# Kernel optimization log

Hardware: AMD Instinct MI355X
Metric: run time of the kernel (lower is better)

Reference implementation:

```python
import jax, jax.numpy as jnp
import numpy as np

B, L, D_IN = 16, 2048, 512
HID, H = 512, 8
D = HID // H          # head dim
FACTOR = 5
U = min(FACTOR * int(np.ceil(np.log(L))), L)  # u_q == u_k == 40 (L == S)


def setup_inputs() -> dict:
    key = jax.random.key(0)
    ks = jax.random.split(key, 8)
    s = 1.0 / np.sqrt(D_IN).astype(np.float32)
    return {
        "q_in": jax.random.normal(ks[0], (B, L, D_IN), jnp.float32),
        "k_in": jax.random.normal(ks[1], (B, L, D_IN), jnp.float32),
        "v_in": jax.random.normal(ks[2], (B, L, D_IN), jnp.float32),
        "Wq": jax.random.normal(ks[3], (D_IN, HID), jnp.float32) * s,
        "Wk": jax.random.normal(ks[4], (D_IN, HID), jnp.float32) * s,
        "Wv": jax.random.normal(ks[5], (D_IN, HID), jnp.float32) * s,
        "Wo": jax.random.normal(ks[6], (HID, HID // H), jnp.float32) / np.sqrt(HID).astype(np.float32),
        "indx_q_seq": jax.random.randint(ks[7], (L,), 0, L, dtype=jnp.int32),
    }


def reference(q_in, k_in, v_in, Wq, Wk, Wv, Wo, indx_q_seq):
    # projections + (memory-reinterpreting, as in the TF source) head reshape
    q = (q_in @ Wq).reshape(B, H, L, D)
    k = (k_in @ Wk).reshape(B, H, L, D)
    v = (v_in @ Wv).reshape(B, H, L, D)

    # --- _prob_qk ---
    # TF's chained gathers on the broadcast k_expand collapse to pairing
    # query s with the single key indx_q_seq[s]; all sample_k columns of
    # Q_K_sample are identical, so M = max - sum/L = dot * (1 - U/L).
    k_sel = k[:, :, indx_q_seq, :]                        # [B,H,L,D]
    dot = jnp.einsum('bhle,bhle->bhl', q, k_sel)          # [B,H,L]
    M = dot - dot * (jnp.float32(U) / jnp.float32(L))
    _, m_top = jax.lax.top_k(M, U)                        # [B,H,U]

    b_idx = jnp.arange(B)[:, None, None]
    h_idx = jnp.arange(H)[None, :, None]
    q_red = q[b_idx, h_idx, m_top]                        # [B,H,U,D]
    scores = jnp.einsum('bhue,bhle->bhul', q_red, k)      # [B,H,U,L]
    scores = scores * (1.0 / np.sqrt(D).astype(np.float32))

    # --- initial context: causal cumsum of values ---
    context = jnp.cumsum(v, axis=-2)                      # [B,H,L,D]

    # --- update context at the top-U query positions (causal mask) ---
    causal = jnp.arange(L)[None, None, None, :] > m_top[..., None]
    scores = jnp.where(causal, -jnp.inf, scores)
    attn = jax.nn.softmax(scores, axis=-1)                # [B,H,U,L]
    upd = jnp.einsum('bhul,bhld->bhud', attn, v)          # [B,H,U,D]
    context = context.at[b_idx, h_idx, m_top].set(upd)

    out = context.reshape(B, L, HID) @ Wo                 # [B,L,HID//H]
    return out
```

## Files before the change

### kernel.cpp

```cpp
#include <hip/hip_runtime.h>
#include <hip/hip_bf16.h>
#include <math.h>

#define B_   16
#define L_   2048
#define DIN  512
#define HID_ 512
#define H_   8
#define D_   64
#define U_   40
#define BH   (B_*H_)

typedef unsigned short u16;
typedef unsigned int u32;
typedef unsigned long long u64;
typedef __bf16 bf16x8 __attribute__((ext_vector_type(8)));
typedef float f32x4 __attribute__((ext_vector_type(4)));

__device__ __forceinline__ u16 f2bf(float x) {
  __bf16 b = (__bf16)x;
  return __builtin_bit_cast(unsigned short, b);
}
__device__ __forceinline__ float bf2f(u16 h) {
  return __uint_as_float(((unsigned)h) << 16);
}
__device__ __forceinline__ float bflo(u32 x) { return __uint_as_float(x << 16); }
__device__ __forceinline__ float bfhi(u32 x) { return __uint_as_float(x & 0xFFFF0000u); }
__device__ __forceinline__ u32 pk2(float a, float b) {
  return (u32)f2bf(a) | ((u32)f2bf(b) << 16);
}
__device__ __forceinline__ void gload16(const u16* g, u16* l) {
  __builtin_amdgcn_global_load_lds(
      (__attribute__((address_space(1))) void*)(g),
      (__attribute__((address_space(3))) void*)(l), 16, 0, 0);
}
__device__ __forceinline__ u64 mkkey(float Mv, int l) {
  u32 fb = __float_as_uint(Mv);
  u32 mapped = (fb & 0x80000000u) ? ~fb : (fb | 0x80000000u);
  return ((u64)mapped << 32) | (u64)(0xFFFFFFFFu - (u32)l);
}

__global__ __launch_bounds__(256)
void wsplit_kernel(const float* __restrict__ W, u16* __restrict__ Bt) {
  int tid = blockIdx.x * 256 + threadIdx.x;
  int n = tid & 511, k = tid >> 9;
  float a = W[(size_t)k * 512 + n];
  u16 hi = f2bf(a);
  u16 lo = f2bf(a - bf2f(hi));
  int kb = k >> 5, kc = k & 31;
  int slotH = kc >> 3, wi = kc & 7;
  int swzH = (slotH     ^ (n & 7)) << 3;
  int swzL = ((4+slotH) ^ (n & 7)) << 3;
  Bt[(size_t)n * 1024 + kb * 64 + swzH + wi] = hi;
  Bt[(size_t)n * 1024 + kb * 64 + swzL + wi] = lo;
}

template<int NPASS>
__global__ __launch_bounds__(256, 4)
void gemm_proj(const float* __restrict__ A, const u16* __restrict__ Bt,
               float* __restrict__ C) {
  __shared__ u16 As[128 * 64];
  __shared__ u16 Bs[128 * 64];
  const int t = threadIdx.x;
  const int w = t >> 6, lane = t & 63;
  const int lhi = lane >> 4, l16 = lane & 15;
  const int row0 = blockIdx.x * 128, col0 = blockIdx.y * 128;
  const int wrow = (w >> 1) * 64, wcol = (w & 1) * 64;

  const u16* gB = Bt + (size_t)(col0 + w * 32 + (lane >> 3)) * 1024 + (lane & 7) * 8;
  u16* lB = &Bs[(w * 32) * 64];

  f32x4 acc[4][4];
  #pragma unroll
  for (int i = 0; i < 4; ++i)
    #pragma unroll
    for (int j = 0; j < 4; ++j) acc[i][j] = (f32x4){0.f, 0.f, 0.f, 0.f};

  for (int kb = 0; kb < 16; ++kb) {
    #pragma unroll
    for (int i = 0; i < 4; ++i)
      gload16(gB + kb * 64 + (size_t)i * 8 * 1024, lB + i * 8 * 64);
    #pragma unroll
    for (int i = 0; i < 4; ++i) {
      int r  = (t >> 3) + 32 * i;
      int c4 = (t & 7) * 4;
      float4 v = *reinterpret_cast<const float4*>(
          &A[(size_t)(row0 + r) * 512 + kb * 32 + c4]);
      ushort4 h4;
      h4.x = f2bf(v.x); h4.y = f2bf(v.y); h4.z = f2bf(v.z); h4.w = f2bf(v.w);
      int slotH = c4 >> 3, wi = c4 & 7;
      int baseH = r * 64 + (((slotH)     ^ (r & 7)) << 3) + wi;
      *reinterpret_cast<ushort4*>(&As[baseH]) = h4;
      if constexpr (NPASS == 3) {
        ushort4 lo4;
        lo4.x = f2bf(v.x - bf2f(h4.x)); lo4.y = f2bf(v.y - bf2f(h4.y));
        lo4.z = f2bf(v.z - bf2f(h4.z)); lo4.w = f2bf(v.w - bf2f(h4.w));
        int baseL = r * 64 + (((4 + slotH) ^ (r & 7)) << 3) + wi;
        *reinterpret_cast<ushort4*>(&As[baseL]) = lo4;
      }
    }
    __syncthreads();

#define PASS(APART, BPART)                                                      \
    { bf16x8 af[4], bfr[4];                                                     \
      _Pragma("unroll") for (int i = 0; i < 4; ++i) {                           \
        int ra = wrow + i * 16 + l16;                                           \
        af[i] = *reinterpret_cast<const bf16x8*>(                               \
            &As[ra * 64 + ((((APART) + lhi) ^ (ra & 7)) << 3)]); }              \
      _Pragma("unroll") for (int j = 0; j < 4; ++j) {                           \
        int cb = wcol + j * 16 + l16;                                           \
        bfr[j] = *reinterpret_cast<const bf16x8*>(                              \
            &Bs[cb * 64 + ((((BPART) + lhi) ^ (cb & 7)) << 3)]); }              \
      _Pragma("unroll") for (int i = 0; i < 4; ++i)                             \
        _Pragma("unroll") for (int j = 0; j < 4; ++j)                           \
          acc[i][j] = __builtin_amdgcn_mfma_f32_16x16x32_bf16(                  \
              af[i], bfr[j], acc[i][j], 0, 0, 0); }

    PASS(0, 0)
    if constexpr (NPASS == 3) {
      PASS(0, 4)
      PASS(4, 0)
    }
#undef PASS
    __syncthreads();
  }
  #pragma unroll
  for (int i = 0; i < 4; ++i)
    #pragma unroll
    for (int j = 0; j < 4; ++j)
      #pragma unroll
      for (int r = 0; r < 4; ++r)
        C[(size_t)(row0 + wrow + i * 16 + lhi * 4 + r) * 512
          + col0 + wcol + j * 16 + l16] = acc[i][j][r];
}

__global__ __launch_bounds__(256)
void dotsel_kernel(const float* __restrict__ qp, const float* __restrict__ kp,
                   const int* __restrict__ indx, u64* __restrict__ cand) {
  __shared__ u64 keys[256];
  __shared__ u64 wmax[4];
  const int bh = blockIdx.x, ch = blockIdx.y;
  const int t = threadIdx.x, w = t >> 6, lane = t & 63;
  const size_t boff = (size_t)bh * 131072;
  const int l0 = ch * 256 + w * 64;
  const float cUL = 40.0f / 2048.0f;

  for (int i = 0; i < 64; i += 4) {
    float p[4];
    #pragma unroll
    for (int jj = 0; jj < 4; ++jj) {
      int l = l0 + i + jj;
      int ls = indx[l];
      p[jj] = qp[boff + (size_t)l * 64 + lane] * kp[boff + (size_t)ls * 64 + lane];
    }
    #pragma unroll
    for (int off = 32; off >= 1; off >>= 1)
      #pragma unroll
      for (int jj = 0; jj < 4; ++jj) p[jj] += __shfl_xor(p[jj], off, 64);
    if (lane == 0) {
      #pragma unroll
      for (int jj = 0; jj < 4; ++jj) {
        float Mv = p[jj] - p[jj] * cUL;
        keys[w * 64 + i + jj] = mkkey(Mv, l0 + i + jj);
      }
    }
  }
  __syncthreads();

  u64 myk = keys[t];
  for (int u = 0; u < U_; ++u) {
    u64 b = myk;
    #pragma unroll
    for (int off = 32; off >= 1; off >>= 1) {
      u64 v = __shfl_xor(b, off, 64);
      if (v > b) b = v;
    }
    if (lane == 0) wmax[w] = b;
    __syncthreads();
    u64 m = wmax[0];
    if (wmax[1] > m) m = wmax[1];
    if (wmax[2] > m) m = wmax[2];
    if (wmax[3] > m) m = wmax[3];
    if (myk == m) myk = 0;
    if (t == 0) cand[((size_t)(bh * 8 + ch)) * U_ + u] = m;
    __syncthreads();
  }
}

__global__ __launch_bounds__(64)
void merge_topk(const u64* __restrict__ cand, int* __restrict__ mtop) {
  const int bh = blockIdx.x;
  const int lane = threadIdx.x;
  u64 c0 = cand[(size_t)bh * 320 + 0 * 64 + lane];
  u64 c1 = cand[(size_t)bh * 320 + 1 * 64 + lane];
  u64 c2 = cand[(size_t)bh * 320 + 2 * 64 + lane];
  u64 c3 = cand[(size_t)bh * 320 + 3 * 64 + lane];
  u64 c4 = cand[(size_t)bh * 320 + 4 * 64 + lane];
  for (int u = 0; u < U_; ++u) {
    u64 b = c0;
    if (c1 > b) b = c1;
    if (c2 > b) b = c2;
    if (c3 > b) b = c3;
    if (c4 > b) b = c4;
    #pragma unroll
    for (int off = 32; off >= 1; off >>= 1) {
      u64 v = __shfl_xor(b, off, 64);
      if (v > b) b = v;
    }
    if (c0 == b) c0 = 0;
    if (c1 == b) c1 = 0;
    if (c2 == b) c2 = 0;
    if (c3 == b) c3 = 0;
    if (c4 == b) c4 = 0;
    if (lane == 0) mtop[bh * U_ + u] = (int)(0xFFFFFFFFu - (u32)b);
  }
}

__global__ __launch_bounds__(256)
void gather_q_kernel(const float* __restrict__ qp, const int* __restrict__ mtop,
                     u16* __restrict__ qredbf) {
  int tid = blockIdx.x * 256 + threadIdx.x;
  int s = tid >> 6;
  int d = tid & 63;
  int bh = s / 48;
  int u = s - bh * 48;
  float val = 0.f;
  if (u < U_) {
    int m = mtop[bh * U_ + u];
    val = qp[(size_t)bh * (L_ * D_) + (size_t)m * D_ + d] * 0.125f;
  }
  qredbf[tid] = f2bf(val);
}

__global__ __launch_bounds__(256)
void scores_mfma(const u16* __restrict__ qredbf, const float* __restrict__ kp,
                 const int* __restrict__ mtop, u16* __restrict__ S) {
  __shared__ u16 As[48 * 64];
  __shared__ u16 Bs[128 * 64];
  __shared__ int ms[U_];
  const int bh = blockIdx.x;
  const int l0 = blockIdx.y * 128;
  const int t = threadIdx.x, w = t >> 6, lane = t & 63;
  const int lhi = lane >> 4, l16 = lane & 15;

  for (int e = t; e < 384; e += 256) {
    int r = e >> 3, s = e & 7;
    *reinterpret_cast<uint4*>(&As[r * 64 + ((s ^ (r & 7)) << 3)]) =
        *reinterpret_cast<const uint4*>(&qredbf[(size_t)bh * 3072 + e * 8]);
  }
  #pragma unroll
  for (int ee = 0; ee < 4; ++ee) {
    int e = t + ee * 256;
    int r = e >> 3, s = e & 7;
    const float* src = &kp[(size_t)bh * 131072 + (size_t)(l0 + r) * 64 + s * 8];
    float4 va = *reinterpret_cast<const float4*>(src);
    float4 vb = *reinterpret_cast<const float4*>(src + 4);
    uint4 w4 = make_uint4(pk2(va.x, va.y), pk2(va.z, va.w),
                          pk2(vb.x, vb.y), pk2(vb.z, vb.w));
    *reinterpret_cast<uint4*>(&Bs[r * 64 + ((s ^ (r & 7)) << 3)]) = w4;
  }
  if (t < U_) ms[t] = mtop[bh * U_ + t];
  __syncthreads();

  f32x4 acc[3][2];
  #pragma unroll
  for (int m = 0; m < 3; ++m)
    #pragma unroll
    for (int n = 0; n < 2; ++n) acc[m][n] = (f32x4){0.f, 0.f, 0.f, 0.f};

  #pragma unroll
  for (int ks = 0; ks < 2; ++ks) {
    bf16x8 a[3], b[2];
    #pragma unroll
    for (int m = 0; m < 3; ++m) {
      int r = m * 16 + l16;
      a[m] = *reinterpret_cast<const bf16x8*>(
          &As[r * 64 + (((ks * 4 + lhi) ^ (r & 7)) << 3)]);
    }
    #pragma unroll
    for (int n = 0; n < 2; ++n) {
      int cb = w * 32 + n * 16 + l16;
      b[n] = *reinterpret_cast<const bf16x8*>(
          &Bs[cb * 64 + (((ks * 4 + lhi) ^ (cb & 7)) << 3)]);
    }
    #pragma unroll
    for (int m = 0; m < 3; ++m)
      #pragma unroll
      for (int n = 0; n < 2; ++n)
        acc[m][n] = __builtin_amdgcn_mfma_f32_16x16x32_bf16(a[m], b[n], acc[m][n], 0, 0, 0);
  }

  #pragma unroll
  for (int m = 0; m < 3; ++m)
    #pragma unroll
    for (int n = 0; n < 2; ++n)
      #pragma unroll
      for (int r = 0; r < 4; ++r) {
        int u = m * 16 + lhi * 4 + r;
        if (u < U_) {
          int l = l0 + w * 32 + n * 16 + l16;
          float val = acc[m][n][r];
          if (l > ms[u]) val = -INFINITY;
          S[((size_t)bh * 48 + u) * 2048 + l] = f2bf(val);
        }
      }
}

__global__ __launch_bounds__(256)
void softmax_kernel(u16* __restrict__ S) {
  __shared__ float red[4];
  const int rr = blockIdx.x;
  const int bh = rr / U_;
  const int u = rr - bh * U_;
  const int t = threadIdx.x;
  uint4* rp = reinterpret_cast<uint4*>(&S[((size_t)bh * 48 + u) * 2048]);
  uint4 raw = rp[t];
  float f[8];
  f[0] = bflo(raw.x); f[1] = bfhi(raw.x); f[2] = bflo(raw.y); f[3] = bfhi(raw.y);
  f[4] = bflo(raw.z); f[5] = bfhi(raw.z); f[6] = bflo(raw.w); f[7] = bfhi(raw.w);
  float m = f[0];
  #pragma unroll
  for (int i = 1; i < 8; ++i) m = fmaxf(m, f[i]);
  #pragma unroll
  for (int off = 32; off >= 1; off >>= 1) m = fmaxf(m, __shfl_xor(m, off, 64));
  if ((t & 63) == 0) red[t >> 6] = m;
  __syncthreads();
  m = fmaxf(fmaxf(red[0], red[1]), fmaxf(red[2], red[3]));
  __syncthreads();
  float s = 0.f;
  #pragma unroll
  for (int i = 0; i < 8; ++i) { f[i] = expf(f[i] - m); s += f[i]; }
  #pragma unroll
  for (int off = 32; off >= 1; off >>= 1) s += __shfl_xor(s, off, 64);
  if ((t & 63) == 0) red[t >> 6] = s;
  __syncthreads();
  s = red[0] + red[1] + red[2] + red[3];
  float inv = 1.0f / s;
  uint4 o;
  o.x = pk2(f[0] * inv, f[1] * inv);
  o.y = pk2(f[2] * inv, f[3] * inv);
  o.z = pk2(f[4] * inv, f[5] * inv);
  o.w = pk2(f[6] * inv, f[7] * inv);
  rp[t] = o;
}

__global__ __launch_bounds__(256)
void pv_mfma(const u16* __restrict__ Pbf, const float* __restrict__ vp,
             float* __restrict__ partial) {
  __shared__ u16 Ps[48 * 128];
  __shared__ u16 Vs[64 * 128];
  const int bh = blockIdx.x, kh = blockIdx.y;
  const int t = threadIdx.x, w = t >> 6, lane = t & 63;
  const int lhi = lane >> 4, l16 = lane & 15;
  const size_t vbase = (size_t)bh * 131072;
  f32x4 acc[3];
  #pragma unroll
  for (int m = 0; m < 3; ++m) acc[m] = (f32x4){0.f, 0.f, 0.f, 0.f};

  for (int ch = 0; ch < 2; ++ch) {
    const int lb = kh * 256 + ch * 128;
    for (int e = t; e < 768; e += 256) {
      int r = e >> 4, s = e & 15;
      int sw = (s & 8) | ((s & 7) ^ (r & 7));
      *reinterpret_cast<uint4*>(&Ps[r * 128 + (sw << 3)]) =
          *reinterpret_cast<const uint4*>(&Pbf[((size_t)bh * 48 + r) * 2048 + lb + s * 8]);
    }
    #pragma unroll
    for (int j = 0; j < 16; ++j) {
      int ll = w * 32 + 2 * j;
      float a = vp[vbase + (size_t)(lb + ll) * 64 + lane];
      float b = vp[vbase + (size_t)(lb + ll + 1) * 64 + lane];
      u32 pk = pk2(a, b);
      int s = ll >> 3;
      int sw = (s & 8) | ((s & 7) ^ (lane & 7));
      *reinterpret_cast<u32*>(&Vs[lane * 128 + (sw << 3) + (ll & 7)]) = pk;
    }
    __syncthreads();
    #pragma unroll
    for (int ks = 0; ks < 4; ++ks) {
      bf16x8 b;
      { int cb = w * 16 + l16; int s = ks * 4 + lhi;
        int sw = (s & 8) | ((s & 7) ^ (cb & 7));
        b = *reinterpret_cast<const bf16x8*>(&Vs[cb * 128 + (sw << 3)]); }
      #pragma unroll
      for (int m = 0; m < 3; ++m) {
        int r = m * 16 + l16; int s = ks * 4 + lhi;
        int sw = (s & 8) | ((s & 7) ^ (r & 7));
        bf16x8 a = *reinterpret_cast<const bf16x8*>(&Ps[r * 128 + (sw << 3)]);
        acc[m] = __builtin_amdgcn_mfma_f32_16x16x32_bf16(a, b, acc[m], 0, 0, 0);
      }
    }
    __syncthreads();
  }
  #pragma unroll
  for (int m = 0; m < 3; ++m)
    #pragma unroll
    for (int r = 0; r < 4; ++r) {
      int u = m * 16 + lhi * 4 + r;
      partial[(((size_t)kh * 128 + bh) * 48 + u) * 64 + w * 16 + l16] = acc[m][r];
    }
}

__global__ __launch_bounds__(256)
void cumsumA(const float* __restrict__ vp, float* __restrict__ seg32) {
  int bh = blockIdx.x, sg = blockIdx.y;
  int t = threadIdx.x, w = t >> 6, lane = t & 63;
  int g = sg * 4 + w;
  size_t base = (size_t)bh * 131072 + (size_t)g * 32 * 64;
  float s = 0.f;
  for (int i = 0; i < 32; ++i) s += vp[base + i * 64 + lane];
  seg32[((size_t)bh * 64 + g) * 64 + lane] = s;
}
__global__ __launch_bounds__(256)
void cumsumB(const float* __restrict__ vp, const float* __restrict__ seg32,
             float* __restrict__ ctx) {
  int bh = blockIdx.x, sg = blockIdx.y;
  int t = threadIdx.x, w = t >> 6, lane = t & 63;
  int g = sg * 4 + w;
  float run = 0.f;
  for (int s = 0; s < g; ++s) run += seg32[((size_t)bh * 64 + s) * 64 + lane];
  size_t base = (size_t)bh * 131072 + (size_t)g * 32 * 64;
  for (int i = 0; i < 32; ++i) {
    run += vp[base + i * 64 + lane];
    ctx[base + i * 64 + lane] = run;
  }
}

__global__ __launch_bounds__(256)
void scatter_kernel(const float* __restrict__ partial, const int* __restrict__ mtop,
                    float* __restrict__ ctx) {
  int tid = blockIdx.x * 256 + threadIdx.x;
  int s = tid >> 6;
  if (s >= BH * U_) return;
  int d = tid & 63;
  int bh = s / U_;
  int u = s - bh * U_;
  float a = 0.f;
  #pragma unroll
  for (int c = 0; c < 8; ++c)
    a += partial[(((size_t)(c * 128 + bh)) * 48 + u) * 64 + d];
  ctx[(size_t)bh * 131072 + (size_t)mtop[s] * 64 + d] = a;
}

__global__ __launch_bounds__(256)
void wo_prep(const float* __restrict__ Wo, u16* __restrict__ WoT) {
  int tid = blockIdx.x * 256 + threadIdx.x;
  int j = tid >> 9, k = tid & 511;
  float v = Wo[(size_t)k * 64 + j];
  int k0 = k & ~63, ko = k & 63;
  int ks = ko >> 5, kc = ko & 31;
  int slot = (ks * 4 + (kc >> 3)) ^ (j & 7);
  WoT[(size_t)j * 512 + k0 + (slot << 3) + (kc & 7)] = f2bf(v);
}

__global__ __launch_bounds__(256, 6)
void gemm_out(const float* __restrict__ ctx, const u16* __restrict__ WoT,
              float* __restrict__ out) {
  __shared__ u16 As[64 * 64];
  __shared__ u16 Bs[64 * 64];
  const int t = threadIdx.x, w = t >> 6, lane = t & 63;
  const int lhi = lane >> 4, l16 = lane & 15;
  const int row0 = blockIdx.x * 64;
  f32x4 acc[4];
  #pragma unroll
  for (int j = 0; j < 4; ++j) acc[j] = (f32x4){0.f, 0.f, 0.f, 0.f};

  for (int k0 = 0; k0 < 512; k0 += 64) {
    #pragma unroll
    for (int ii = 0; ii < 2; ++ii) {
      int e = t + ii * 256;
      int j = e >> 3, s = e & 7;
      gload16(WoT + (size_t)j * 512 + k0 + s * 8, Bs + (size_t)(w * 64 + ii * 256) * 8);
    }
    #pragma unroll
    for (int ii = 0; ii < 2; ++ii) {
      int e = t + ii * 256;
      int r = e >> 3, s = e & 7;
      const float* src = &ctx[(size_t)(row0 + r) * 512 + k0 + s * 8];
      float4 va = *reinterpret_cast<const float4*>(src);
      float4 vb = *reinterpret_cast<const float4*>(src + 4);
      uint4 w4 = make_uint4(pk2(va.x, va.y), pk2(va.z, va.w),
                            pk2(vb.x, vb.y), pk2(vb.z, vb.w));
      *reinterpret_cast<uint4*>(&As[r * 64 + ((s ^ (r & 7)) << 3)]) = w4;
    }
    __syncthreads();
    #pragma unroll
    for (int ks = 0; ks < 2; ++ks) {
      int r = w * 16 + l16;
      bf16x8 a = *reinterpret_cast<const bf16x8*>(
          &As[r * 64 + (((ks * 4 + lhi) ^ (r & 7)) << 3)]);
      #pragma unroll
      for (int jf = 0; jf < 4; ++jf) {
        int cb = jf * 16 + l16;
        bf16x8 b = *reinterpret_cast<const bf16x8*>(
            &Bs[cb * 64 + (((ks * 4 + lhi) ^ (cb & 7)) << 3)]);
        acc[jf] = __builtin_amdgcn_mfma_f32_16x16x32_bf16(a, b, acc[jf], 0, 0, 0);
      }
    }
    __syncthreads();
  }
  #pragma unroll
  for (int jf = 0; jf < 4; ++jf)
    #pragma unroll
    for (int r = 0; r < 4; ++r)
      out[(size_t)(row0 + w * 16 + lhi * 4 + r) * 64 + jf * 16 + l16] = acc[jf][r];
}

extern "C" void kernel_launch(void* const* d_in, const int* in_sizes, int n_in,
                              void* d_out, int out_size, void* d_ws, size_t ws_size,
                              hipStream_t stream) {
  const float* q_in = (const float*)d_in[0];
  const float* k_in = (const float*)d_in[1];
  const float* v_in = (const float*)d_in[2];
  const float* Wq   = (const float*)d_in[3];
  const float* Wk   = (const float*)d_in[4];
  const float* Wv   = (const float*)d_in[5];
  const float* Wo   = (const float*)d_in[6];
  const int*   indx = (const int*)d_in[7];
  float* out = (float*)d_out;

  float* ws = (float*)d_ws;
  float* qp   = ws;
  float* kp   = ws + 16777216;
  float* vp   = ws + 33554432;
  u16*   Bt   = (u16*)(ws + 50331648);
  u64*   cand = (u64*)Bt;
  u16*   WoT  = (u16*)Bt;
  u16*   qredbf = (u16*)(ws + 50593792);
  int*   mtop = (int*)(ws + 50921472);
  u16*   S    = (u16*)qp;
  float* ctx  = qp;
  float* partial = kp;
  float* seg32   = kp + 3145728;

  const int M = B_ * L_;

  wsplit_kernel<<<1024, 256, 0, stream>>>(Wq, Bt);
  gemm_proj<3><<<dim3(M / 128, 4), 256, 0, stream>>>(q_in, Bt, qp);
  wsplit_kernel<<<1024, 256, 0, stream>>>(Wk, Bt);
  gemm_proj<3><<<dim3(M / 128, 4), 256, 0, stream>>>(k_in, Bt, kp);
  wsplit_kernel<<<1024, 256, 0, stream>>>(Wv, Bt);
  gemm_proj<1><<<dim3(M / 128, 4), 256, 0, stream>>>(v_in, Bt, vp);

  dotsel_kernel<<<dim3(BH, 8), 256, 0, stream>>>(qp, kp, indx, cand);
  merge_topk<<<BH, 64, 0, stream>>>(cand, mtop);
  gather_q_kernel<<<(BH * 48 * 64) / 256, 256, 0, stream>>>(qp, mtop, qredbf);

  scores_mfma<<<dim3(BH, 16), 256, 0, stream>>>(qredbf, kp, mtop, S);
  softmax_kernel<<<BH * U_, 256, 0, stream>>>(S);
  pv_mfma<<<dim3(BH, 8), 256, 0, stream>>>(S, vp, partial);

  cumsumA<<<dim3(BH, 16), 256, 0, stream>>>(vp, seg32);
  cumsumB<<<dim3(BH, 16), 256, 0, stream>>>(vp, seg32, ctx);

  scatter_kernel<<<(BH * U_ * 64) / 256, 256, 0, stream>>>(partial, mtop, ctx);

  wo_prep<<<128, 256, 0, stream>>>(Wo, WoT);
  gemm_out<<<M / 64, 256, 0, stream>>>(ctx, WoT, out);
}
```

Measured before the change: 374.6 us.

## Reorder split-bf16 MFMA loads, vectorize dot selection, double-buffer top-k reduction

The GEMM inner loop now loads the B fragments (high and low parts) once and streams A rows one at a time, replacing three separate passes that each reloaded fragments from LDS. This lowers register pressure and LDS traffic. The dot-product selection kernel now computes four rows per wave with float4 loads and a 16-lane shuffle reduction instead of scalar loads with 64-lane reductions. The iterative top-k double-buffers the per-wave max array so one barrier per iteration can be removed.

```diff
diff --git a/kernel.cpp b/kernel.cpp
--- a/kernel.cpp
+++ b/kernel.cpp
@@ -101,27 +101,35 @@
     }
     __syncthreads();
 
-#define PASS(APART, BPART)                                                      \
-    { bf16x8 af[4], bfr[4];                                                     \
-      _Pragma("unroll") for (int i = 0; i < 4; ++i) {                           \
-        int ra = wrow + i * 16 + l16;                                           \
-        af[i] = *reinterpret_cast<const bf16x8*>(                               \
-            &As[ra * 64 + ((((APART) + lhi) ^ (ra & 7)) << 3)]); }              \
-      _Pragma("unroll") for (int j = 0; j < 4; ++j) {                           \
-        int cb = wcol + j * 16 + l16;                                           \
-        bfr[j] = *reinterpret_cast<const bf16x8*>(                              \
-            &Bs[cb * 64 + ((((BPART) + lhi) ^ (cb & 7)) << 3)]); }              \
-      _Pragma("unroll") for (int i = 0; i < 4; ++i)                             \
-        _Pragma("unroll") for (int j = 0; j < 4; ++j)                           \
-          acc[i][j] = __builtin_amdgcn_mfma_f32_16x16x32_bf16(                  \
-              af[i], bfr[j], acc[i][j], 0, 0, 0); }
-
-    PASS(0, 0)
-    if constexpr (NPASS == 3) {
-      PASS(0, 4)
-      PASS(4, 0)
-    }
-#undef PASS
+    bf16x8 bfH[4], bfL[4];
+    #pragma unroll
+    for (int j = 0; j < 4; ++j) {
+      int cb = wcol + j * 16 + l16;
+      bfH[j] = *reinterpret_cast<const bf16x8*>(
+          &Bs[cb * 64 + ((lhi ^ (cb & 7)) << 3)]);
+      if constexpr (NPASS == 3)
+        bfL[j] = *reinterpret_cast<const bf16x8*>(
+            &Bs[cb * 64 + (((4 + lhi) ^ (cb & 7)) << 3)]);
+    }
+    #pragma unroll
+    for (int i = 0; i < 4; ++i) {
+      int ra = wrow + i * 16 + l16;
+      bf16x8 aH = *reinterpret_cast<const bf16x8*>(
+          &As[ra * 64 + ((lhi ^ (ra & 7)) << 3)]);
+      #pragma unroll
+      for (int j = 0; j < 4; ++j)
+        acc[i][j] = __builtin_amdgcn_mfma_f32_16x16x32_bf16(aH, bfH[j], acc[i][j], 0, 0, 0);
+      if constexpr (NPASS == 3) {
+        bf16x8 aL = *reinterpret_cast<const bf16x8*>(
+            &As[ra * 64 + (((4 + lhi) ^ (ra & 7)) << 3)]);
+        #pragma unroll
+        for (int j = 0; j < 4; ++j)
+          acc[i][j] = __builtin_amdgcn_mfma_f32_16x16x32_bf16(aH, bfL[j], acc[i][j], 0, 0, 0);
+        #pragma unroll
+        for (int j = 0; j < 4; ++j)
+          acc[i][j] = __builtin_amdgcn_mfma_f32_16x16x32_bf16(aL, bfH[j], acc[i][j], 0, 0, 0);
+      }
+    }
     __syncthreads();
   }
   #pragma unroll
@@ -138,31 +146,29 @@
 void dotsel_kernel(const float* __restrict__ qp, const float* __restrict__ kp,
                    const int* __restrict__ indx, u64* __restrict__ cand) {
   __shared__ u64 keys[256];
-  __shared__ u64 wmax[4];
+  __shared__ u64 wmax[2][4];
   const int bh = blockIdx.x, ch = blockIdx.y;
   const int t = threadIdx.x, w = t >> 6, lane = t & 63;
   const size_t boff = (size_t)bh * 131072;
   const int l0 = ch * 256 + w * 64;
   const float cUL = 40.0f / 2048.0f;
-
-  for (int i = 0; i < 64; i += 4) {
-    float p[4];
-    #pragma unroll
-    for (int jj = 0; jj < 4; ++jj) {
-      int l = l0 + i + jj;
-      int ls = indx[l];
-      p[jj] = qp[boff + (size_t)l * 64 + lane] * kp[boff + (size_t)ls * 64 + lane];
-    }
-    #pragma unroll
-    for (int off = 32; off >= 1; off >>= 1)
-      #pragma unroll
-      for (int jj = 0; jj < 4; ++jj) p[jj] += __shfl_xor(p[jj], off, 64);
-    if (lane == 0) {
-      #pragma unroll
-      for (int jj = 0; jj < 4; ++jj) {
-        float Mv = p[jj] - p[jj] * cUL;
-        keys[w * 64 + i + jj] = mkkey(Mv, l0 + i + jj);
-      }
+  const int li = lane >> 4;
+  const int dq = lane & 15;
+
+  #pragma unroll 4
+  for (int i = 0; i < 16; ++i) {
+    int l = l0 + i * 4 + li;
+    int ls = indx[l];
+    float4 q4 = *reinterpret_cast<const float4*>(&qp[boff + (size_t)l * 64 + dq * 4]);
+    float4 k4 = *reinterpret_cast<const float4*>(&kp[boff + (size_t)ls * 64 + dq * 4]);
+    float p = q4.x * k4.x + q4.y * k4.y + q4.z * k4.z + q4.w * k4.w;
+    p += __shfl_xor(p, 1, 64);
+    p += __shfl_xor(p, 2, 64);
+    p += __shfl_xor(p, 4, 64);
+    p += __shfl_xor(p, 8, 64);
+    if (dq == 0) {
+      float Mv = p - p * cUL;
+      keys[w * 64 + i * 4 + li] = mkkey(Mv, l);
     }
   }
   __syncthreads();
@@ -175,15 +181,15 @@
       u64 v = __shfl_xor(b, off, 64);
       if (v > b) b = v;
     }
-    if (lane == 0) wmax[w] = b;
-    __syncthreads();
-    u64 m = wmax[0];
-    if (wmax[1] > m) m = wmax[1];
-    if (wmax[2] > m) m = wmax[2];
-    if (wmax[3] > m) m = wmax[3];
+    if (lane == 0) wmax[u & 1][w] = b;
+    __syncthreads();
+    const u64* wm = wmax[u & 1];
+    u64 m = wm[0];
+    if (wm[1] > m) m = wm[1];
+    if (wm[2] > m) m = wm[2];
+    if (wm[3] > m) m = wm[3];
     if (myk == m) myk = 0;
     if (t == 0) cand[((size_t)(bh * 8 + ch)) * U_ + u] = m;
-    __syncthreads();
   }
 }
 
```

New measurement: 364.6 us. 2.7% less time.
